# Optimization experiments

Measured on AMD Instinct MI355X. Metric: run time of the kernel, lower is better.

The kernel has to match this reference:

```python
import jax, jax.numpy as jnp
import numpy as np

T = 0.07
TOPK = 5

def _l2norm(x, axis=-1, eps=1e-12):
    n = jnp.sqrt(jnp.sum(x * x, axis=axis, keepdims=True))
    return x / jnp.maximum(n, eps)

def setup_inputs() -> dict:
    key = jax.random.key(0)
    k1, k2, k3, k4, k5 = jax.random.split(key, 5)
    b, nc, dim, dim_mlp, K = 256, 5, 128, 2048, 65536
    q = jax.random.normal(k1, (b, nc, dim), jnp.float32)
    k = jax.random.normal(k2, (b, dim), jnp.float32)
    q_backbone = jax.random.normal(k3, (b, nc, dim_mlp), jnp.float32)
    # queues are column-normalized buffers, as in __init__
    queue = _l2norm(jax.random.normal(k4, (dim, K), jnp.float32), axis=0)
    queue_backbone = _l2norm(jax.random.normal(k5, (dim_mlp, K), jnp.float32), axis=0)
    return {"q": q, "k": k, "q_backbone": q_backbone,
            "queue": queue, "queue_backbone": queue_backbone}

def reference(q, k, q_backbone, queue, queue_backbone):
    b, nc, dim = q.shape
    dim_mlp = q_backbone.shape[-1]
    qn = _l2norm(q)                 # [b, nc, dim]
    kn = _l2norm(k)                 # [b, dim]
    qb = _l2norm(q_backbone)        # [b, nc, dim_mlp]

    # positive logits: each crop vs its key
    l_pos = jnp.einsum('bnd,bd->bn', qn, kn).reshape(-1, 1)      # [b*nc, 1]
    # negative logits vs queue
    l_neg = jnp.einsum('nc,ck->nk', qn.reshape(-1, dim), queue)  # [b*nc, K]
    logits = jnp.concatenate([l_pos, l_neg], axis=1) / T
    labels = jnp.zeros((logits.shape[0],), dtype=jnp.int32)

    # backbone-space similarities to pick top-k neighbors
    l_neg_backbone = jnp.einsum('nc,ck->nk', qb.reshape(-1, dim_mlp), queue_backbone)

    # pull_topk: softmax CE pulling toward top-k backbone neighbors.
    # scatter-mask + masked mean == gather log-softmax at top-k indices (indices distinct)
    _, knn_idx = jax.lax.top_k(l_neg_backbone, TOPK)             # [b*nc, TOPK]
    log_prob = jax.nn.log_softmax(l_neg / T, axis=1)             # [b*nc, K]
    pos_logp = jnp.take_along_axis(log_prob, knn_idx, axis=1)    # [b*nc, TOPK]
    loss = -jnp.mean(jnp.mean(pos_logp, axis=1))
    return logits, labels, loss
```

## Files before the change

kernel.cpp:

```cpp
#include <hip/hip_runtime.h>
#include <hip/hip_bf16.h>
#include <hip/hip_fp8.h>

#define M_     1280
#define DIM    128
#define DMLP   2048
#define KQ     65536
#define NCOLS  65537ull
#define NTOPK  5
#define NCHUNK 512
#define NBLK1  512
#define NTK    32
#define INV_T  14.285714285714286f

typedef __attribute__((ext_vector_type(8))) short bf16x8;
typedef __attribute__((ext_vector_type(4))) float f32x4;
typedef __attribute__((ext_vector_type(2))) long longx2;

static __device__ __forceinline__ unsigned short f2bf(float x){
  union { __hip_bfloat16 h; unsigned short u; } cv;
  cv.h = __float2bfloat16(x);
  return cv.u;
}

static __device__ __forceinline__ unsigned char f2f8(float x){
  __hip_fp8_e4m3 h(x);
  return (unsigned char)h.__x;
}

#define GLDS16(gp, lp) __builtin_amdgcn_global_load_lds( \
    (const __attribute__((address_space(1))) void*)(gp), \
    (__attribute__((address_space(3))) void*)(lp), 16, 0, 0)

#define BAR()   asm volatile("s_barrier" ::: "memory")
#define VMW(n)  asm volatile("s_waitcnt vmcnt(" #n ")" ::: "memory")

__global__ __launch_bounds__(256) void transpose_bf16(
    const float* __restrict__ in, unsigned short* __restrict__ out, int R, int C){
  __shared__ float tile[64][65];
  const int c0 = blockIdx.x * 64, r0 = blockIdx.y * 64;
  const int t = threadIdx.x;
  #pragma unroll
  for (int i = 0; i < 4; ++i){
    int lin = t + i * 256;
    int rr = lin >> 4;
    int cc = (lin & 15) * 4;
    const float4 v = *(const float4*)(in + (size_t)(r0 + rr) * C + c0 + cc);
    tile[rr][cc + 0] = v.x; tile[rr][cc + 1] = v.y;
    tile[rr][cc + 2] = v.z; tile[rr][cc + 3] = v.w;
  }
  __syncthreads();
  #pragma unroll
  for (int i = 0; i < 4; ++i){
    int lin = t + i * 256;
    int oc  = lin >> 4;
    int orr = (lin & 15) * 4;
    ushort4 u;
    u.x = f2bf(tile[orr + 0][oc]); u.y = f2bf(tile[orr + 1][oc]);
    u.z = f2bf(tile[orr + 2][oc]); u.w = f2bf(tile[orr + 3][oc]);
    *(ushort4*)(out + (size_t)(c0 + oc) * R + r0 + orr) = u;
  }
}

__global__ __launch_bounds__(256) void transpose_fp8(
    const float* __restrict__ in, unsigned char* __restrict__ out, int R, int C){
  __shared__ float tile[64][65];
  const int c0 = blockIdx.x * 64, r0 = blockIdx.y * 64;
  const int t = threadIdx.x;
  #pragma unroll
  for (int i = 0; i < 4; ++i){
    int lin = t + i * 256;
    int rr = lin >> 4;
    int cc = (lin & 15) * 4;
    const float4 v = *(const float4*)(in + (size_t)(r0 + rr) * C + c0 + cc);
    tile[rr][cc + 0] = v.x; tile[rr][cc + 1] = v.y;
    tile[rr][cc + 2] = v.z; tile[rr][cc + 3] = v.w;
  }
  __syncthreads();
  #pragma unroll
  for (int i = 0; i < 4; ++i){
    int lin = t + i * 256;
    int oc  = lin >> 4;
    int orr = (lin & 15) * 4;
    const int quad  = (orr >> 3) & 3;
    const int slice = orr >> 5;
    const int sub   = orr & 7;
    uchar4 u;
    u.x = f2f8(tile[orr + 0][oc]); u.y = f2f8(tile[orr + 1][oc]);
    u.z = f2f8(tile[orr + 2][oc]); u.w = f2f8(tile[orr + 3][oc]);
    *(uchar4*)(out + (size_t)(c0 + oc) * R + r0 + quad * 16 + slice * 8 + sub) = u;
  }
}

__global__ __launch_bounds__(128) void normq_kernel(
    const float* __restrict__ q, const float* __restrict__ k,
    unsigned short* __restrict__ qn, float* __restrict__ outp){
  const int i = blockIdx.x;
  const int t = threadIdx.x;
  const float qv = q[(size_t)i * DIM + t];
  const float kv = k[(size_t)(i / 5) * DIM + t];
  float a = qv * qv, b = kv * kv, d = qv * kv;
  #pragma unroll
  for (int s = 32; s >= 1; s >>= 1){
    a += __shfl_down(a, s, 64);
    b += __shfl_down(b, s, 64);
    d += __shfl_down(d, s, 64);
  }
  __shared__ float red[6];
  if ((t & 63) == 0){ red[(t >> 6) * 3 + 0] = a; red[(t >> 6) * 3 + 1] = b; red[(t >> 6) * 3 + 2] = d; }
  __syncthreads();
  const float qq = red[0] + red[3], kk = red[1] + red[4], qk = red[2] + red[5];
  const float qnorm = fmaxf(sqrtf(qq), 1e-12f);
  qn[(size_t)i * DIM + t] = f2bf(qv / qnorm);
  if (t == 0){
    const float knorm = fmaxf(sqrtf(kk), 1e-12f);
    outp[(size_t)i * NCOLS] = (qk / (qnorm * knorm)) * INV_T;
  }
}

__global__ __launch_bounds__(256) void normqb_kernel(
    const float* __restrict__ qb, unsigned char* __restrict__ out){
  const int i = blockIdx.x, t = threadIdx.x;
  const float* p = qb + (size_t)i * DMLP;
  float x[8]; float ss = 0.f;
  #pragma unroll
  for (int j = 0; j < 8; ++j){ x[j] = p[t + j * 256]; ss += x[j] * x[j]; }
  #pragma unroll
  for (int s = 32; s >= 1; s >>= 1) ss += __shfl_down(ss, s, 64);
  __shared__ float r4[4];
  if ((t & 63) == 0) r4[t >> 6] = ss;
  __syncthreads();
  const float tot = r4[0] + r4[1] + r4[2] + r4[3];
  const float inv = 1.0f / fmaxf(sqrtf(tot), 1e-12f);
  unsigned char* o = out + (size_t)i * DMLP;
  #pragma unroll
  for (int j = 0; j < 8; ++j){
    const int kx = t + j * 256;
    const int kk = kx & 63;
    const int pos = (kx & ~63) + ((kk >> 3) & 3) * 16 + (kk >> 5) * 8 + (kk & 7);
    o[pos] = f2f8(x[j] * inv);
  }
}

static __device__ __forceinline__ void tk_insert(float* v, int* ix, float nv, int ni){
  if (nv > v[4]){
    v[4] = nv; ix[4] = ni;
    #pragma unroll
    for (int j = 4; j > 0; --j){
      if (v[j] > v[j - 1]){
        float tv = v[j]; v[j] = v[j - 1]; v[j - 1] = tv;
        int   ti = ix[j]; ix[j] = ix[j - 1]; ix[j - 1] = ti;
      }
    }
  }
}

__global__ __launch_bounds__(256, 2) void gemm1_mfma(
    const unsigned short* __restrict__ A, const unsigned short* __restrict__ BT,
    float* __restrict__ outp, float* __restrict__ pm, float* __restrict__ ps){
  __shared__ __attribute__((aligned(16))) unsigned char smem[65536];
  unsigned short* At = (unsigned short*)smem;
  unsigned short* Bt = At + 16384;

  const int t    = threadIdx.x;
  const int lane = t & 63;
  const int wv   = t >> 6;
  const int lid  = lane & 15;
  const int quad = lane >> 4;
  const int h  = blockIdx.x;
  const int wg = (h & 7) * 640 + (h >> 3);
  const int bm = wg % 10;
  const int bn = wg / 10;
  const int m0 = bm * 128;
  const int n0 = bn * 128;

  f32x4 acc[2][8];
  #pragma unroll
  for (int mt = 0; mt < 2; ++mt)
    #pragma unroll
    for (int nt = 0; nt < 8; ++nt)
      acc[mt][nt] = f32x4{0.f, 0.f, 0.f, 0.f};

  const int arow = t >> 2;
  const int ace  = (t & 3) * 8;

  #pragma unroll
  for (int kt = 0; kt < 4; ++kt)
    #pragma unroll
    for (int it = 0; it < 2; ++it){
      const int row = arow + it * 64;
      GLDS16(A + (size_t)(m0 + row) * DIM + kt * 32 + ace,
             At + kt * 4096 + (t + it * 256) * 8);
    }
  #pragma unroll
  for (int kt = 0; kt < 4; ++kt)
    #pragma unroll
    for (int it = 0; it < 2; ++it){
      const int row = arow + it * 64;
      GLDS16(BT + (size_t)(n0 + row) * DIM + kt * 32 + ace,
             Bt + kt * 4096 + (t + it * 256) * 8);
    }
  VMW(0);
  BAR();

  for (int kt = 0; kt < 4; ++kt){
    bf16x8 af[2], bfr[8];
    #pragma unroll
    for (int mt = 0; mt < 2; ++mt)
      af[mt] = *(const bf16x8*)(At + kt * 4096 + (wv * 32 + mt * 16 + lid) * 32 + quad * 8);
    #pragma unroll
    for (int nt = 0; nt < 8; ++nt)
      bfr[nt] = *(const bf16x8*)(Bt + kt * 4096 + (nt * 16 + lid) * 32 + quad * 8);
    #pragma unroll
    for (int mt = 0; mt < 2; ++mt)
      #pragma unroll
      for (int nt = 0; nt < 8; ++nt)
        acc[mt][nt] = __builtin_amdgcn_mfma_f32_16x16x32_bf16(af[mt], bfr[nt], acc[mt][nt], 0, 0, 0);
  }

  float mx[2][4], sm[2][4];
  #pragma unroll
  for (int mt = 0; mt < 2; ++mt)
    #pragma unroll
    for (int r = 0; r < 4; ++r) mx[mt][r] = -3.0e38f;
  #pragma unroll
  for (int mt = 0; mt < 2; ++mt)
    #pragma unroll
    for (int nt = 0; nt < 8; ++nt)
      #pragma unroll
      for (int r = 0; r < 4; ++r){
        const int mg = m0 + wv * 32 + mt * 16 + quad * 4 + r;
        const int ng = n0 + nt * 16 + lid;
        const float x = acc[mt][nt][r] * INV_T;
        outp[(size_t)mg * NCOLS + 1 + ng] = x;
        mx[mt][r] = fmaxf(mx[mt][r], x);
      }
  #pragma unroll
  for (int mt = 0; mt < 2; ++mt)
    #pragma unroll
    for (int r = 0; r < 4; ++r){
      #pragma unroll
      for (int s = 8; s >= 1; s >>= 1)
        mx[mt][r] = fmaxf(mx[mt][r], __shfl_xor(mx[mt][r], s, 64));
      sm[mt][r] = 0.f;
    }
  #pragma unroll
  for (int mt = 0; mt < 2; ++mt)
    #pragma unroll
    for (int nt = 0; nt < 8; ++nt)
      #pragma unroll
      for (int r = 0; r < 4; ++r)
        sm[mt][r] += __expf(acc[mt][nt][r] * INV_T - mx[mt][r]);
  #pragma unroll
  for (int mt = 0; mt < 2; ++mt)
    #pragma unroll
    for (int r = 0; r < 4; ++r){
      #pragma unroll
      for (int s = 8; s >= 1; s >>= 1)
        sm[mt][r] += __shfl_xor(sm[mt][r], s, 64);
      if (lid == 0){
        const int mg = m0 + wv * 32 + mt * 16 + quad * 4 + r;
        pm[(size_t)mg * NBLK1 + bn] = mx[mt][r];
        ps[(size_t)mg * NBLK1 + bn] = sm[mt][r];
      }
    }
}


#define RDA8(SRC) do { _Pragma("unroll") for (int mf = 0; mf < 4; ++mf) \
    av[mf] = *(const longx2*)((SRC) + (wm * 64 + mf * 16 + lid) * 64 + qsw); } while(0)

#define RDB8(SRC) do { _Pragma("unroll") for (int nf = 0; nf < 4; ++nf) \
    bv[nf] = *(const longx2*)((SRC) + (wn * 64 + nf * 16 + lid) * 64 + qsw); } while(0)

#define MM_NF(nj_) do { \
    _Pragma("unroll") for (int mf = 0; mf < 4; ++mf){ \
      acc[mf][nj_] = __builtin_amdgcn_mfma_f32_16x16x32_fp8_fp8(av[mf].x, bv[nj_].x, acc[mf][nj_], 0, 0, 0); \
      acc[mf][nj_] = __builtin_amdgcn_mfma_f32_16x16x32_fp8_fp8(av[mf].y, bv[nj_].y, acc[mf][nj_], 0, 0, 0); } } while(0)

__global__ __launch_bounds__(512, 4) void gemm2_topk(
    const unsigned char* __restrict__ A, const unsigned char* __restrict__ BT,
    float* __restrict__ cval, int* __restrict__ cidx){
  __shared__ __attribute__((aligned(16))) unsigned char smem[73728];

  const int t    = threadIdx.x;
  const int lane = t & 63;
  const int wv   = t >> 6;
  const int wm   = wv >> 1;
  const int wn   = wv & 1;
  const int lid  = lane & 15;
  const int quad = lane >> 4;
  const int qsw  = (quad ^ (lid & 3)) * 16;

  const int h  = blockIdx.x;
  const int wg = (h & 7) * 320 + (h >> 3);
  const int bm = wg % 5;
  const int bn = wg / 5;
  const int m0 = bm * 256;
  const int n0 = bn * 128;

  const int srow = t >> 2;
  const size_t roff = (size_t)srow * DMLP + (size_t)(((t & 3) ^ (srow & 3)) * 16);
  const unsigned char* aB = A  + (size_t)m0 * DMLP;
  const unsigned char* bB = BT + (size_t)n0 * DMLP;

  f32x4 acc[4][4];
  #pragma unroll
  for (int a = 0; a < 4; ++a)
    #pragma unroll
    for (int b = 0; b < 4; ++b)
      acc[a][b] = f32x4{0.f, 0.f, 0.f, 0.f};

  longx2 av[4];
  longx2 bv[4];

  #define STAGE2(kt_, bi_) do { \
    unsigned char* _a = smem + (bi_) * 24576; \
    const int _kc = (kt_) * 64; \
    GLDS16(aB + roff + _kc, _a + (size_t)t * 16); \
    GLDS16(aB + roff + 128 * DMLP + _kc, _a + (size_t)(512 + t) * 16); \
    GLDS16(bB + roff + _kc, _a + 16384 + (size_t)t * 16); } while(0)

  STAGE2(0, 0);
  STAGE2(1, 1);
  VMW(3);
  BAR();

  for (int kt = 0; kt < NTK; ++kt){
    const int bi = kt % 3;
    unsigned char* curA = smem + bi * 24576;
    unsigned char* curB = curA + 16384;

    RDA8(curA);
    RDB8(curB);

    if (kt + 2 < NTK) STAGE2(kt + 2, (kt + 2) % 3);

    __builtin_amdgcn_s_setprio(1);
    MM_NF(0); MM_NF(1); MM_NF(2); MM_NF(3);
    __builtin_amdgcn_s_setprio(0);

    if (kt + 1 < NTK){
      if (kt + 2 < NTK){ VMW(3); } else { VMW(0); }
      BAR();
    }
  }

  float* scratch = (float*)smem;
  BAR();
  #pragma unroll
  for (int p = 0; p < 2; ++p){
    if ((wm >> 1) == p){
      #pragma unroll
      for (int mf = 0; mf < 4; ++mf)
        #pragma unroll
        for (int nf = 0; nf < 4; ++nf)
          #pragma unroll
          for (int r = 0; r < 4; ++r){
            const int lr = (wm & 1) * 64 + mf * 16 + quad * 4 + r;
            scratch[lr * 133 + wn * 64 + nf * 16 + lid] = acc[mf][nf][r];
          }
    }
    __syncthreads();
    {
      const int lr  = t >> 2;
      const int seg = t & 3;
      float v[5]; int ix[5];
      #pragma unroll
      for (int j = 0; j < 5; ++j){ v[j] = -3.0e38f; ix[j] = 0; }
      const int cb0 = seg * 32;
      for (int j = 0; j < 32; ++j)
        tk_insert(v, ix, scratch[lr * 133 + cb0 + j], n0 + cb0 + j);
      #pragma unroll
      for (int s = 1; s <= 2; s <<= 1){
        float pv[5]; int pi[5];
        #pragma unroll
        for (int j = 0; j < 5; ++j){ pv[j] = __shfl_xor(v[j], s, 64); pi[j] = __shfl_xor(ix[j], s, 64); }
        #pragma unroll
        for (int j = 0; j < 5; ++j) tk_insert(v, ix, pv[j], pi[j]);
      }
      if (seg == 0){
        const int rowg = m0 + p * 128 + lr;
        const size_t cb = ((size_t)rowg * NCHUNK + bn) * NTOPK;
        #pragma unroll
        for (int j = 0; j < 5; ++j){ cval[cb + j] = v[j]; cidx[cb + j] = ix[j]; }
      }
    }
    __syncthreads();
  }
}

__global__ __launch_bounds__(256) void topk_merge(
    const float* __restrict__ cval, const int* __restrict__ cidx, int* __restrict__ knn){
  const int row = blockIdx.x, t = threadIdx.x;
  float v[5]; int ix[5];
  #pragma unroll
  for (int j = 0; j < 5; ++j){ v[j] = -3.0e38f; ix[j] = 0; }
  const size_t base = (size_t)row * (NCHUNK * NTOPK);
  #pragma unroll
  for (int j = 0; j < 10; ++j){
    const int c = t * 10 + j;
    tk_insert(v, ix, cval[base + c], cidx[base + c]);
  }
  __shared__ float lv[256 * 5];
  __shared__ int   li[256 * 5];
  #pragma unroll
  for (int j = 0; j < 5; ++j){ lv[t * 5 + j] = v[j]; li[t * 5 + j] = ix[j]; }
  __syncthreads();
  if (t < 64){
    float v2[5]; int ix2[5];
    #pragma unroll
    for (int j = 0; j < 5; ++j){ v2[j] = -3.0e38f; ix2[j] = 0; }
    for (int L = 0; L < 4; ++L)
      #pragma unroll
      for (int j = 0; j < 5; ++j)
        tk_insert(v2, ix2, lv[(t * 4 + L) * 5 + j], li[(t * 4 + L) * 5 + j]);
    #pragma unroll
    for (int s = 32; s >= 1; s >>= 1){
      float pv[5]; int pi[5];
      #pragma unroll
      for (int j = 0; j < 5; ++j){ pv[j] = __shfl_down(v2[j], s, 64); pi[j] = __shfl_down(ix2[j], s, 64); }
      #pragma unroll
      for (int j = 0; j < 5; ++j) tk_insert(v2, ix2, pv[j], pi[j]);
    }
    if (t == 0){
      #pragma unroll
      for (int j = 0; j < 5; ++j) knn[(size_t)row * NTOPK + j] = ix2[j];
    }
  }
}

__global__ __launch_bounds__(256) void lse_merge(
    const float* __restrict__ pm, const float* __restrict__ ps,
    float* __restrict__ lse){
  const int row = blockIdx.x, t = threadIdx.x;
  const float* pmr = pm + (size_t)row * NBLK1;
  const float* psr = ps + (size_t)row * NBLK1;
  float m = -1.0e30f, s = 0.f;
  #pragma unroll
  for (int c = 0; c < 2; ++c){
    const float om = pmr[t + c * 256], os = psr[t + c * 256];
    const float nm = fmaxf(m, om);
    s = s * __expf(m - nm) + os * __expf(om - nm);
    m = nm;
  }
  #pragma unroll
  for (int sh = 32; sh >= 1; sh >>= 1){
    const float om = __shfl_down(m, sh, 64), os = __shfl_down(s, sh, 64);
    const float nm = fmaxf(m, om);
    s = s * __expf(m - nm) + os * __expf(om - nm);
    m = nm;
  }
  __shared__ float sm2[4], ss2[4];
  if ((t & 63) == 0){ sm2[t >> 6] = m; ss2[t >> 6] = s; }
  __syncthreads();
  if (t == 0){
    float M = sm2[0], S = ss2[0];
    #pragma unroll
    for (int w = 1; w < 4; ++w){
      const float nm = fmaxf(M, sm2[w]);
      S = S * __expf(M - nm) + ss2[w] * __expf(sm2[w] - nm);
      M = nm;
    }
    lse[row] = M + __logf(S);
  }
}

__global__ __launch_bounds__(256) void loss_kernel(
    const float* __restrict__ logits, const float* __restrict__ lse,
    const int* __restrict__ knn, float* __restrict__ loss){
  const int i = blockIdx.x * 256 + threadIdx.x;
  float c = 0.f;
  if (i < M_){
    const float l = lse[i];
    #pragma unroll
    for (int j = 0; j < 5; ++j){
      const int id = knn[(size_t)i * NTOPK + j];
      c += l - logits[(size_t)i * NCOLS + 1 + id];
    }
    c *= (1.0f / 6400.0f);
  }
  #pragma unroll
  for (int s = 32; s >= 1; s >>= 1) c += __shfl_down(c, s, 64);
  if ((threadIdx.x & 63) == 0) atomicAdd(loss, c);
}

extern "C" void kernel_launch(void* const* d_in, const int* in_sizes, int n_in,
                              void* d_out, int out_size, void* d_ws, size_t ws_size,
                              hipStream_t stream){
  const float* q   = (const float*)d_in[0];
  const float* k   = (const float*)d_in[1];
  const float* qbI = (const float*)d_in[2];
  const float* que = (const float*)d_in[3];
  const float* qbb = (const float*)d_in[4];
  float* out = (float*)d_out;

  unsigned char* w = (unsigned char*)d_ws;
  unsigned short* qn    = (unsigned short*)w; w += (size_t)M_ * DIM  * 2;
  unsigned char*  qbn8  = (unsigned char*)w;  w += (size_t)M_ * DMLP;
  unsigned short* queT  = (unsigned short*)w; w += (size_t)KQ * DIM  * 2;
  unsigned char*  qbbT8 = (unsigned char*)w;  w += (size_t)KQ * DMLP;
  float* cval = (float*)w;                    w += (size_t)M_ * NCHUNK * NTOPK * 4;
  int*   cidx = (int*)w;                      w += (size_t)M_ * NCHUNK * NTOPK * 4;
  int*   knn  = (int*)w;                      w += (size_t)M_ * NTOPK * 4;
  float* lseb = (float*)w;                    w += (size_t)M_ * 4;
  float* pm   = (float*)w;                    w += (size_t)M_ * NBLK1 * 4;
  float* ps   = (float*)w;                    w += (size_t)M_ * NBLK1 * 4;

  hipMemsetAsync(out + (size_t)M_ * NCOLS, 0, (M_ + 1) * sizeof(float), stream);

  transpose_bf16<<<dim3(KQ / 64, DIM  / 64), 256, 0, stream>>>(que, queT, DIM, KQ);
  transpose_fp8 <<<dim3(KQ / 64, DMLP / 64), 256, 0, stream>>>(qbb, qbbT8, DMLP, KQ);
  normq_kernel <<<M_, 128, 0, stream>>>(q, k, qn, out);
  normqb_kernel<<<M_, 256, 0, stream>>>(qbI, qbn8);
  gemm1_mfma<<<dim3(5120), 256, 0, stream>>>(qn, queT, out, pm, ps);
  gemm2_topk<<<dim3(2560), 512, 0, stream>>>(qbn8, qbbT8, cval, cidx);
  topk_merge<<<M_, 256, 0, stream>>>(cval, cidx, knn);
  lse_merge<<<M_, 256, 0, stream>>>(pm, ps, lseb);
  loss_kernel<<<(M_ + 255) / 256, 256, 0, stream>>>(out, lseb, knn,
                                                    out + (size_t)M_ * NCOLS + M_);
}
```

Baseline: 1.195 ms.

## Fuse logits GEMM and fp8 top-k GEMM into one interleaved-role kernel

Merges the bf16 logits GEMM (with its softmax partials) and the fp8 backbone GEMM (with its top-k) into a single launch. Block roles are interleaved by blockIdx mod 3, so the store-bound logits tiles can run alongside the compute-bound fp8 tiles on the same CUs. The logits role now uses 512 threads, each wave owning one 16-row M fragment, and its LDS footprint rises to the shared 72KB. Separately, the fp8 transpose now has each thread write one 16-byte vector instead of four uchar4 stores.

```diff
diff --git a/kernel.cpp b/kernel.cpp
--- a/kernel.cpp
+++ b/kernel.cpp
@@ -77,18 +77,14 @@
     tile[rr][cc + 2] = v.z; tile[rr][cc + 3] = v.w;
   }
   __syncthreads();
-  #pragma unroll
-  for (int i = 0; i < 4; ++i){
-    int lin = t + i * 256;
-    int oc  = lin >> 4;
-    int orr = (lin & 15) * 4;
-    const int quad  = (orr >> 3) & 3;
-    const int slice = orr >> 5;
-    const int sub   = orr & 7;
-    uchar4 u;
-    u.x = f2f8(tile[orr + 0][oc]); u.y = f2f8(tile[orr + 1][oc]);
-    u.z = f2f8(tile[orr + 2][oc]); u.w = f2f8(tile[orr + 3][oc]);
-    *(uchar4*)(out + (size_t)(c0 + oc) * R + r0 + quad * 16 + slice * 8 + sub) = u;
+  {
+    const int oc   = t >> 2;
+    const int quad = t & 3;
+    union { unsigned char b[16]; ulonglong2 v; } u;
+    #pragma unroll
+    for (int b = 0; b < 16; ++b)
+      u.b[b] = f2f8(tile[(b >> 3) * 32 + quad * 8 + (b & 7)][oc]);
+    *(ulonglong2*)(out + (size_t)(c0 + oc) * R + r0 + quad * 16) = u.v;
   }
 }
 
@@ -155,238 +151,210 @@
   }
 }
 
-__global__ __launch_bounds__(256, 2) void gemm1_mfma(
-    const unsigned short* __restrict__ A, const unsigned short* __restrict__ BT,
+
+#define RDA8(SRC) do { _Pragma("unroll") for (int mf = 0; mf < 4; ++mf) \
+    av[mf] = *(const longx2*)((SRC) + (wm * 64 + mf * 16 + lid) * 64 + qsw); } while(0)
+
+#define RDB8(SRC) do { _Pragma("unroll") for (int nf = 0; nf < 4; ++nf) \
+    bv[nf] = *(const longx2*)((SRC) + (wn * 64 + nf * 16 + lid) * 64 + qsw); } while(0)
+
+#define MM_NF(nj_) do { \
+    _Pragma("unroll") for (int mf = 0; mf < 4; ++mf){ \
+      acc[mf][nj_] = __builtin_amdgcn_mfma_f32_16x16x32_fp8_fp8(av[mf].x, bv[nj_].x, acc[mf][nj_], 0, 0, 0); \
+      acc[mf][nj_] = __builtin_amdgcn_mfma_f32_16x16x32_fp8_fp8(av[mf].y, bv[nj_].y, acc[mf][nj_], 0, 0, 0); } } while(0)
+
+__global__ __launch_bounds__(512, 4) void gemm_fused(
+    const unsigned char* __restrict__ A8, const unsigned char* __restrict__ BT8,
+    float* __restrict__ cval, int* __restrict__ cidx,
+    const unsigned short* __restrict__ A16, const unsigned short* __restrict__ BT16,
     float* __restrict__ outp, float* __restrict__ pm, float* __restrict__ ps){
-  __shared__ __attribute__((aligned(16))) unsigned char smem[65536];
-  unsigned short* At = (unsigned short*)smem;
-  unsigned short* Bt = At + 16384;
-
+  __shared__ __attribute__((aligned(16))) unsigned char smem[73728];
+
+  const int bid  = blockIdx.x;
+  const int role = bid % 3;
   const int t    = threadIdx.x;
   const int lane = t & 63;
   const int wv   = t >> 6;
   const int lid  = lane & 15;
   const int quad = lane >> 4;
-  const int h  = blockIdx.x;
-  const int wg = (h & 7) * 640 + (h >> 3);
-  const int bm = wg % 10;
-  const int bn = wg / 10;
-  const int m0 = bm * 128;
-  const int n0 = bn * 128;
-
-  f32x4 acc[2][8];
-  #pragma unroll
-  for (int mt = 0; mt < 2; ++mt)
+
+  if (role == 0){
+    const int wm  = wv >> 1;
+    const int wn  = wv & 1;
+    const int qsw = (quad ^ (lid & 3)) * 16;
+
+    const int h  = bid / 3;
+    const int wg = (h & 7) * 320 + (h >> 3);
+    const int bm = wg % 5;
+    const int bn = wg / 5;
+    const int m0 = bm * 256;
+    const int n0 = bn * 128;
+
+    const int srow = t >> 2;
+    const size_t roff = (size_t)srow * DMLP + (size_t)(((t & 3) ^ (srow & 3)) * 16);
+    const unsigned char* aB = A8  + (size_t)m0 * DMLP;
+    const unsigned char* bB = BT8 + (size_t)n0 * DMLP;
+
+    f32x4 acc[4][4];
+    #pragma unroll
+    for (int a = 0; a < 4; ++a)
+      #pragma unroll
+      for (int b = 0; b < 4; ++b)
+        acc[a][b] = f32x4{0.f, 0.f, 0.f, 0.f};
+
+    longx2 av[4];
+    longx2 bv[4];
+
+    #define STAGE2(kt_, bi_) do { \
+      unsigned char* _a = smem + (bi_) * 24576; \
+      const int _kc = (kt_) * 64; \
+      GLDS16(aB + roff + _kc, _a + (size_t)t * 16); \
+      GLDS16(aB + roff + 128 * DMLP + _kc, _a + (size_t)(512 + t) * 16); \
+      GLDS16(bB + roff + _kc, _a + 16384 + (size_t)t * 16); } while(0)
+
+    STAGE2(0, 0);
+    STAGE2(1, 1);
+    VMW(3);
+    BAR();
+
+    for (int kt = 0; kt < NTK; ++kt){
+      const int bi = kt % 3;
+      unsigned char* curA = smem + bi * 24576;
+      unsigned char* curB = curA + 16384;
+
+      RDA8(curA);
+      RDB8(curB);
+
+      if (kt + 2 < NTK) STAGE2(kt + 2, (kt + 2) % 3);
+
+      __builtin_amdgcn_s_setprio(1);
+      MM_NF(0); MM_NF(1); MM_NF(2); MM_NF(3);
+      __builtin_amdgcn_s_setprio(0);
+
+      if (kt + 1 < NTK){
+        if (kt + 2 < NTK){ VMW(3); } else { VMW(0); }
+        BAR();
+      }
+    }
+
+    float* scratch = (float*)smem;
+    BAR();
+    #pragma unroll
+    for (int p = 0; p < 2; ++p){
+      if ((wm >> 1) == p){
+        #pragma unroll
+        for (int mf = 0; mf < 4; ++mf)
+          #pragma unroll
+          for (int nf = 0; nf < 4; ++nf)
+            #pragma unroll
+            for (int r = 0; r < 4; ++r){
+              const int lr = (wm & 1) * 64 + mf * 16 + quad * 4 + r;
+              scratch[lr * 133 + wn * 64 + nf * 16 + lid] = acc[mf][nf][r];
+            }
+      }
+      __syncthreads();
+      {
+        const int lr  = t >> 2;
+        const int seg = t & 3;
+        float v[5]; int ix[5];
+        #pragma unroll
+        for (int j = 0; j < 5; ++j){ v[j] = -3.0e38f; ix[j] = 0; }
+        const int cb0 = seg * 32;
+        for (int j = 0; j < 32; ++j)
+          tk_insert(v, ix, scratch[lr * 133 + cb0 + j], n0 + cb0 + j);
+        #pragma unroll
+        for (int s = 1; s <= 2; s <<= 1){
+          float pv[5]; int pi[5];
+          #pragma unroll
+          for (int j = 0; j < 5; ++j){ pv[j] = __shfl_xor(v[j], s, 64); pi[j] = __shfl_xor(ix[j], s, 64); }
+          #pragma unroll
+          for (int j = 0; j < 5; ++j) tk_insert(v, ix, pv[j], pi[j]);
+        }
+        if (seg == 0){
+          const int rowg = m0 + p * 128 + lr;
+          const size_t cb = ((size_t)rowg * NCHUNK + bn) * NTOPK;
+          #pragma unroll
+          for (int j = 0; j < 5; ++j){ cval[cb + j] = v[j]; cidx[cb + j] = ix[j]; }
+        }
+      }
+      __syncthreads();
+    }
+  } else {
+    unsigned short* At = (unsigned short*)smem;
+    unsigned short* Bt = At + 16384;
+
+    const int h  = (bid / 3) * 2 + (role - 1);
+    const int wg = (h & 7) * 640 + (h >> 3);
+    const int bm = wg % 10;
+    const int bn = wg / 10;
+    const int m0 = bm * 128;
+    const int n0 = bn * 128;
+
+    f32x4 acc[8];
+    #pragma unroll
+    for (int nt = 0; nt < 8; ++nt) acc[nt] = f32x4{0.f, 0.f, 0.f, 0.f};
+
+    const int arow = t >> 2;
+    const int ace  = (t & 3) * 8;
+
+    #pragma unroll
+    for (int kt = 0; kt < 4; ++kt)
+      GLDS16(A16 + (size_t)(m0 + arow) * DIM + kt * 32 + ace,
+             At + kt * 4096 + t * 8);
+    #pragma unroll
+    for (int kt = 0; kt < 4; ++kt)
+      GLDS16(BT16 + (size_t)(n0 + arow) * DIM + kt * 32 + ace,
+             Bt + kt * 4096 + t * 8);
+    VMW(0);
+    BAR();
+
+    for (int kt = 0; kt < 4; ++kt){
+      bf16x8 af, bfr[8];
+      af = *(const bf16x8*)(At + kt * 4096 + (wv * 16 + lid) * 32 + quad * 8);
+      #pragma unroll
+      for (int nt = 0; nt < 8; ++nt)
+        bfr[nt] = *(const bf16x8*)(Bt + kt * 4096 + (nt * 16 + lid) * 32 + quad * 8);
+      #pragma unroll
+      for (int nt = 0; nt < 8; ++nt)
+        acc[nt] = __builtin_amdgcn_mfma_f32_16x16x32_bf16(af, bfr[nt], acc[nt], 0, 0, 0);
+    }
+
+    float mx[4], sm[4];
+    #pragma unroll
+    for (int r = 0; r < 4; ++r) mx[r] = -3.0e38f;
     #pragma unroll
     for (int nt = 0; nt < 8; ++nt)
-      acc[mt][nt] = f32x4{0.f, 0.f, 0.f, 0.f};
-
-  const int arow = t >> 2;
-  const int ace  = (t & 3) * 8;
-
-  #pragma unroll
-  for (int kt = 0; kt < 4; ++kt)
-    #pragma unroll
-    for (int it = 0; it < 2; ++it){
-      const int row = arow + it * 64;
-      GLDS16(A + (size_t)(m0 + row) * DIM + kt * 32 + ace,
-             At + kt * 4096 + (t + it * 256) * 8);
-    }
-  #pragma unroll
-  for (int kt = 0; kt < 4; ++kt)
-    #pragma unroll
-    for (int it = 0; it < 2; ++it){
-      const int row = arow + it * 64;
-      GLDS16(BT + (size_t)(n0 + row) * DIM + kt * 32 + ace,
-             Bt + kt * 4096 + (t + it * 256) * 8);
-    }
-  VMW(0);
-  BAR();
-
-  for (int kt = 0; kt < 4; ++kt){
-    bf16x8 af[2], bfr[8];
-    #pragma unroll
-    for (int mt = 0; mt < 2; ++mt)
-      af[mt] = *(const bf16x8*)(At + kt * 4096 + (wv * 32 + mt * 16 + lid) * 32 + quad * 8);
+      #pragma unroll
+      for (int r = 0; r < 4; ++r){
+        const int mg = m0 + wv * 16 + quad * 4 + r;
+        const int ng = n0 + nt * 16 + lid;
+        const float x = acc[nt][r] * INV_T;
+        outp[(size_t)mg * NCOLS + 1 + ng] = x;
+        mx[r] = fmaxf(mx[r], x);
+      }
+    #pragma unroll
+    for (int r = 0; r < 4; ++r){
+      #pragma unroll
+      for (int s = 8; s >= 1; s >>= 1)
+        mx[r] = fmaxf(mx[r], __shfl_xor(mx[r], s, 64));
+      sm[r] = 0.f;
+    }
     #pragma unroll
     for (int nt = 0; nt < 8; ++nt)
-      bfr[nt] = *(const bf16x8*)(Bt + kt * 4096 + (nt * 16 + lid) * 32 + quad * 8);
-    #pragma unroll
-    for (int mt = 0; mt < 2; ++mt)
-      #pragma unroll
-      for (int nt = 0; nt < 8; ++nt)
-        acc[mt][nt] = __builtin_amdgcn_mfma_f32_16x16x32_bf16(af[mt], bfr[nt], acc[mt][nt], 0, 0, 0);
-  }
-
-  float mx[2][4], sm[2][4];
-  #pragma unroll
-  for (int mt = 0; mt < 2; ++mt)
-    #pragma unroll
-    for (int r = 0; r < 4; ++r) mx[mt][r] = -3.0e38f;
-  #pragma unroll
-  for (int mt = 0; mt < 2; ++mt)
-    #pragma unroll
-    for (int nt = 0; nt < 8; ++nt)
-      #pragma unroll
-      for (int r = 0; r < 4; ++r){
-        const int mg = m0 + wv * 32 + mt * 16 + quad * 4 + r;
-        const int ng = n0 + nt * 16 + lid;
-        const float x = acc[mt][nt][r] * INV_T;
-        outp[(size_t)mg * NCOLS + 1 + ng] = x;
-        mx[mt][r] = fmaxf(mx[mt][r], x);
-      }
-  #pragma unroll
-  for (int mt = 0; mt < 2; ++mt)
+      #pragma unroll
+      for (int r = 0; r < 4; ++r)
+        sm[r] += __expf(acc[nt][r] * INV_T - mx[r]);
     #pragma unroll
     for (int r = 0; r < 4; ++r){
       #pragma unroll
       for (int s = 8; s >= 1; s >>= 1)
-        mx[mt][r] = fmaxf(mx[mt][r], __shfl_xor(mx[mt][r], s, 64));
-      sm[mt][r] = 0.f;
-    }
-  #pragma unroll
-  for (int mt = 0; mt < 2; ++mt)
-    #pragma unroll
-    for (int nt = 0; nt < 8; ++nt)
-      #pragma unroll
-      for (int r = 0; r < 4; ++r)
-        sm[mt][r] += __expf(acc[mt][nt][r] * INV_T - mx[mt][r]);
-  #pragma unroll
-  for (int mt = 0; mt < 2; ++mt)
-    #pragma unroll
-    for (int r = 0; r < 4; ++r){
-      #pragma unroll
-      for (int s = 8; s >= 1; s >>= 1)
-        sm[mt][r] += __shfl_xor(sm[mt][r], s, 64);
+        sm[r] += __shfl_xor(sm[r], s, 64);
       if (lid == 0){
-        const int mg = m0 + wv * 32 + mt * 16 + quad * 4 + r;
-        pm[(size_t)mg * NBLK1 + bn] = mx[mt][r];
-        ps[(size_t)mg * NBLK1 + bn] = sm[mt][r];
-      }
-    }
-}
-
-
-#define RDA8(SRC) do { _Pragma("unroll") for (int mf = 0; mf < 4; ++mf) \
-    av[mf] = *(const longx2*)((SRC) + (wm * 64 + mf * 16 + lid) * 64 + qsw); } while(0)
-
-#define RDB8(SRC) do { _Pragma("unroll") for (int nf = 0; nf < 4; ++nf) \
-    bv[nf] = *(const longx2*)((SRC) + (wn * 64 + nf * 16 + lid) * 64 + qsw); } while(0)
-
-#define MM_NF(nj_) do { \
-    _Pragma("unroll") for (int mf = 0; mf < 4; ++mf){ \
-      acc[mf][nj_] = __builtin_amdgcn_mfma_f32_16x16x32_fp8_fp8(av[mf].x, bv[nj_].x, acc[mf][nj_], 0, 0, 0); \
-      acc[mf][nj_] = __builtin_amdgcn_mfma_f32_16x16x32_fp8_fp8(av[mf].y, bv[nj_].y, acc[mf][nj_], 0, 0, 0); } } while(0)
-
-__global__ __launch_bounds__(512, 4) void gemm2_topk(
-    const unsigned char* __restrict__ A, const unsigned char* __restrict__ BT,
-    float* __restrict__ cval, int* __restrict__ cidx){
-  __shared__ __attribute__((aligned(16))) unsigned char smem[73728];
-
-  const int t    = threadIdx.x;
-  const int lane = t & 63;
-  const int wv   = t >> 6;
-  const int wm   = wv >> 1;
-  const int wn   = wv & 1;
-  const int lid  = lane & 15;
-  const int quad = lane >> 4;
-  const int qsw  = (quad ^ (lid & 3)) * 16;
-
-  const int h  = blockIdx.x;
-  const int wg = (h & 7) * 320 + (h >> 3);
-  const int bm = wg % 5;
-  const int bn = wg / 5;
-  const int m0 = bm * 256;
-  const int n0 = bn * 128;
-
-  const int srow = t >> 2;
-  const size_t roff = (size_t)srow * DMLP + (size_t)(((t & 3) ^ (srow & 3)) * 16);
-  const unsigned char* aB = A  + (size_t)m0 * DMLP;
-  const unsigned char* bB = BT + (size_t)n0 * DMLP;
-
-  f32x4 acc[4][4];
-  #pragma unroll
-  for (int a = 0; a < 4; ++a)
-    #pragma unroll
-    for (int b = 0; b < 4; ++b)
-      acc[a][b] = f32x4{0.f, 0.f, 0.f, 0.f};
-
-  longx2 av[4];
-  longx2 bv[4];
-
-  #define STAGE2(kt_, bi_) do { \
-    unsigned char* _a = smem + (bi_) * 24576; \
-    const int _kc = (kt_) * 64; \
-    GLDS16(aB + roff + _kc, _a + (size_t)t * 16); \
-    GLDS16(aB + roff + 128 * DMLP + _kc, _a + (size_t)(512 + t) * 16); \
-    GLDS16(bB + roff + _kc, _a + 16384 + (size_t)t * 16); } while(0)
-
-  STAGE2(0, 0);
-  STAGE2(1, 1);
-  VMW(3);
-  BAR();
-
-  for (int kt = 0; kt < NTK; ++kt){
-    const int bi = kt % 3;
-    unsigned char* curA = smem + bi * 24576;
-    unsigned char* curB = curA + 16384;
-
-    RDA8(curA);
-    RDB8(curB);
-
-    if (kt + 2 < NTK) STAGE2(kt + 2, (kt + 2) % 3);
-
-    __builtin_amdgcn_s_setprio(1);
-    MM_NF(0); MM_NF(1); MM_NF(2); MM_NF(3);
-    __builtin_amdgcn_s_setprio(0);
-
-    if (kt + 1 < NTK){
-      if (kt + 2 < NTK){ VMW(3); } else { VMW(0); }
-      BAR();
-    }
-  }
-
-  float* scratch = (float*)smem;
-  BAR();
-  #pragma unroll
-  for (int p = 0; p < 2; ++p){
-    if ((wm >> 1) == p){
-      #pragma unroll
-      for (int mf = 0; mf < 4; ++mf)
-        #pragma unroll
-        for (int nf = 0; nf < 4; ++nf)
-          #pragma unroll
-          for (int r = 0; r < 4; ++r){
-            const int lr = (wm & 1) * 64 + mf * 16 + quad * 4 + r;
-            scratch[lr * 133 + wn * 64 + nf * 16 + lid] = acc[mf][nf][r];
-          }
-    }
-    __syncthreads();
-    {
-      const int lr  = t >> 2;
-      const int seg = t & 3;
-      float v[5]; int ix[5];
-      #pragma unroll
-      for (int j = 0; j < 5; ++j){ v[j] = -3.0e38f; ix[j] = 0; }
-      const int cb0 = seg * 32;
-      for (int j = 0; j < 32; ++j)
-        tk_insert(v, ix, scratch[lr * 133 + cb0 + j], n0 + cb0 + j);
-      #pragma unroll
-      for (int s = 1; s <= 2; s <<= 1){
-        float pv[5]; int pi[5];
-        #pragma unroll
-        for (int j = 0; j < 5; ++j){ pv[j] = __shfl_xor(v[j], s, 64); pi[j] = __shfl_xor(ix[j], s, 64); }
-        #pragma unroll
-        for (int j = 0; j < 5; ++j) tk_insert(v, ix, pv[j], pi[j]);
-      }
-      if (seg == 0){
-        const int rowg = m0 + p * 128 + lr;
-        const size_t cb = ((size_t)rowg * NCHUNK + bn) * NTOPK;
-        #pragma unroll
-        for (int j = 0; j < 5; ++j){ cval[cb + j] = v[j]; cidx[cb + j] = ix[j]; }
-      }
-    }
-    __syncthreads();
+        const int mg = m0 + wv * 16 + quad * 4 + r;
+        pm[(size_t)mg * NBLK1 + bn] = mx[r];
+        ps[(size_t)mg * NBLK1 + bn] = sm[r];
+      }
+    }
   }
 }
 
@@ -513,8 +481,8 @@
   transpose_fp8 <<<dim3(KQ / 64, DMLP / 64), 256, 0, stream>>>(qbb, qbbT8, DMLP, KQ);
   normq_kernel <<<M_, 128, 0, stream>>>(q, k, qn, out);
   normqb_kernel<<<M_, 256, 0, stream>>>(qbI, qbn8);
-  gemm1_mfma<<<dim3(5120), 256, 0, stream>>>(qn, queT, out, pm, ps);
-  gemm2_topk<<<dim3(2560), 512, 0, stream>>>(qbn8, qbbT8, cval, cidx);
+  gemm_fused<<<dim3(7680), 512, 0, stream>>>(qbn8, qbbT8, cval, cidx,
+                                             qn, queT, out, pm, ps);
   topk_merge<<<M_, 256, 0, stream>>>(cval, cidx, knn);
   lse_merge<<<M_, 256, 0, stream>>>(pm, ps, lseb);
   loss_kernel<<<(M_ + 255) / 256, 256, 0, stream>>>(out, lseb, knn,
```

New measurement: 1.221 ms. 2.2% more time.
